# Performance work log

Measured on AMD Instinct MI355X. Metric: run time of the kernel, lower is better.

## Reference

```python
import jax, jax.numpy as jnp
import numpy as np

# atom_dict indices
N_IDX, CA_IDX, C_IDX = 0, 1, 2
O4P_IDX, C2P_IDX, C1P_IDX = 11, 14, 15
NA_REF_IDX = 15  # C1'
TOP_K = 30
NUM_RBF = 16
MAX_REL = 32
NUM_POLY = 3
B, L, A = 1, 512, 24


def setup_inputs() -> dict:
    key = jax.random.key(0)
    ks = jax.random.split(key, 8)
    X = 5.0 * jax.random.normal(ks[0], (B, L, A, 3), dtype=jnp.float32)
    mask = jnp.ones((B, L), dtype=jnp.float32)
    R_idx = jnp.broadcast_to(jnp.arange(L, dtype=jnp.int32), (B, L))
    chain_labels = jnp.broadcast_to((jnp.arange(L) // (L // 2)).astype(jnp.int32), (B, L))
    X_m = jnp.ones((B, L, A), dtype=jnp.float32)
    R_polymer_type = jax.random.randint(ks[1], (B, L), 0, NUM_POLY)
    protein_mask = (R_polymer_type == 0).astype(jnp.float32)
    dna_mask = (R_polymer_type == 1).astype(jnp.float32)
    rna_mask = (R_polymer_type == 2).astype(jnp.float32)
    TOTAL_ATOMS = A + 2
    edge_in = 2 * MAX_REL + 2  # placeholder; real edge_in below
    edge_in = NUM_RBF * TOTAL_ATOMS * TOTAL_ATOMS + 16  # 10832
    W_pos = 0.1 * jax.random.normal(ks[2], (16, 2 * MAX_REL + 2), dtype=jnp.float32)
    b_pos = 0.01 * jax.random.normal(ks[3], (16,), dtype=jnp.float32)
    W_edge = 0.02 * jax.random.normal(ks[4], (128, edge_in), dtype=jnp.float32)
    W_node = 0.1 * jax.random.normal(ks[5], (128, NUM_POLY), dtype=jnp.float32)
    gamma_e = jnp.ones((128,), jnp.float32); beta_e = jnp.zeros((128,), jnp.float32)
    gamma_n = jnp.ones((128,), jnp.float32); beta_n = jnp.zeros((128,), jnp.float32)
    return dict(X=X, mask=mask, R_idx=R_idx, chain_labels=chain_labels, X_m=X_m,
                protein_mask=protein_mask, dna_mask=dna_mask, rna_mask=rna_mask,
                R_polymer_type=R_polymer_type, W_pos=W_pos, b_pos=b_pos,
                W_edge=W_edge, W_node=W_node, gamma_e=gamma_e, beta_e=beta_e,
                gamma_n=gamma_n, beta_n=beta_n)


def _get_cb(n, ca, c, wa, wb, wc):
    b = ca - n
    cc = c - ca
    a = jnp.cross(b, cc)
    return wa * a + wb * b + wc * cc + ca


def _layernorm(x, g, b, eps=1e-5):
    m = x.mean(-1, keepdims=True)
    v = ((x - m) ** 2).mean(-1, keepdims=True)
    return (x - m) / jnp.sqrt(v + eps) * g + b


def _dist_topk(Xc, mask):
    # Xc: [B,L,3]
    mask2d = mask[:, None, :] * mask[:, :, None]  # [B,L,L]
    dX = Xc[:, None, :, :] - Xc[:, :, None, :]
    D = mask2d * jnp.sqrt((dX ** 2).sum(-1) + 1e-6)
    D_max = D.max(-1, keepdims=True)
    D_adjust = D + (1.0 - mask2d) * D_max
    negD, E_idx = jax.lax.top_k(-D_adjust, TOP_K)  # smallest distances
    return -negD, E_idx


def reference(X, mask, R_idx, chain_labels, X_m, protein_mask, dna_mask, rna_mask,
              R_polymer_type, W_pos, b_pos, W_edge, W_node, gamma_e, beta_e,
              gamma_n, beta_n):
    Bb, Ll = X.shape[0], X.shape[1]
    Ca = X[:, :, CA_IDX]
    Nb = X[:, :, N_IDX]
    Cc = X[:, :, C_IDX]
    Cb = _get_cb(Nb, Ca, Cc, -0.58273431, 0.56802827, -0.54067466)
    na_ref = X[:, :, NA_REF_IDX]
    N_na = _get_cb(X[:, :, O4P_IDX], X[:, :, C1P_IDX], X[:, :, C2P_IDX],
                   -0.56967352, 0.51055973, -0.53122153)
    aug_X = jnp.concatenate([X, Cb[:, :, None, :], N_na[:, :, None, :]], axis=2)  # [B,L,26,3]
    aug_Xm = jnp.concatenate([X_m, protein_mask[:, :, None],
                              (rna_mask + dna_mask)[:, :, None]], axis=-1)  # [B,L,26]

    _, E_idx = _dist_topk(Ca + na_ref, mask)  # [B,L,K]

    # gather neighbor atoms / masks: [B,L,K,26,3], [B,L,K,26]
    bidx = jnp.arange(Bb)[:, None, None]
    X_g = aug_X[bidx, E_idx]
    Xm_g = aug_Xm[bidx, E_idx]

    # all-atom pairwise distances [B,L,K,26,26]
    Dall = jnp.sqrt(((aug_X[:, :, None, :, None, :] - X_g[:, :, :, None, :, :]) ** 2).sum(-1) + 1e-6)
    D_mu = jnp.linspace(2.0, 22.0, NUM_RBF)
    D_sigma = (22.0 - 2.0) / NUM_RBF
    RBF = jnp.exp(-((Dall[..., None] - D_mu) / D_sigma) ** 2)  # [B,L,K,26,26,16]
    RBF = RBF * aug_Xm[:, :, None, :, None, None] * Xm_g[:, :, :, None, :, None]
    RBF_all = RBF.reshape(Bb, Ll, TOP_K, -1)  # [B,L,K,26*26*16]

    offset = R_idx[:, :, None] - R_idx[:, None, :]  # [B,L,L]
    offset = jnp.take_along_axis(offset, E_idx, axis=2)  # [B,L,K]
    d_chains = (chain_labels[:, :, None] == chain_labels[:, None, :]).astype(jnp.int32)
    E_chains = jnp.take_along_axis(d_chains, E_idx, axis=2)

    d = jnp.clip(offset + MAX_REL, 0, 2 * MAX_REL) * E_chains + (1 - E_chains) * (2 * MAX_REL + 1)
    d_onehot = jax.nn.one_hot(d, 2 * MAX_REL + 2, dtype=jnp.float32)
    E_positional = d_onehot @ W_pos.T + b_pos  # [B,L,K,16]

    E = jnp.concatenate([E_positional, RBF_all], axis=-1)
    E = E @ W_edge.T  # [B,L,K,128]
    E = _layernorm(E, gamma_e, beta_e)

    V = jax.nn.one_hot(R_polymer_type, NUM_POLY, dtype=jnp.float32) @ W_node.T
    V = _layernorm(V, gamma_n, beta_n)
    return V, E, E_idx
```

## Files before the change

kernel.cpp:

```cpp
#include <hip/hip_runtime.h>
#include <stdint.h>


#define NRES   512
#define TOPK   30
#define NATOM  26
#define KTOT   10832
#define NBLK128 85
#define MTOT   (NRES*TOPK)
#define NOUT   128
#define KSPLIT 4
#define TBINS  1024
#define TRANGE 25.6f

#define OFF_AUGX4  0u
#define OFF_EIDX   212992u
#define OFF_WSWZ   274432u
#define OFF_EPART  1667072u
#define OFF_TAB    25260032u

#define OUT_V     0
#define OUT_E     (NRES*NOUT)
#define OUT_EIDX  (OUT_E + MTOT*NOUT)

typedef __attribute__((ext_vector_type(4))) float f32x4;
typedef __attribute__((ext_vector_type(8))) int   i32x8;

#define SA_C    0.96089792702915984f
#define MU0_C   1.9217958540583197f
#define MUS_C   1.2811972360388798f
#define MUS2_C  (MUS_C*MUS_C)
#define SCL1    0x7f7f7f7f
#define TSCL    (SA_C * (float)TBINS / TRANGE)

__device__ __forceinline__ unsigned short f2bf(float f) {
    unsigned u = __builtin_bit_cast(unsigned, f);
    return (unsigned short)((u + 0x7fffu + ((u >> 16) & 1u)) >> 16);
}
__device__ __forceinline__ float bf2f(unsigned short u) {
    return __builtin_bit_cast(float, (unsigned)u << 16);
}
__device__ __forceinline__ float bflo(unsigned u) {
    return __builtin_bit_cast(float, u << 16);
}
__device__ __forceinline__ float bfhi(unsigned u) {
    return __builtin_bit_cast(float, u & 0xffff0000u);
}
__device__ __forceinline__ unsigned long long shfl_xor_u64(unsigned long long v, int m) {
    unsigned lo = (unsigned)v, hi = (unsigned)(v >> 32);
    lo = (unsigned)__shfl_xor((int)lo, m, 64);
    hi = (unsigned)__shfl_xor((int)hi, m, 64);
    return ((unsigned long long)hi << 32) | lo;
}
__device__ __forceinline__ float fexp2(float x) { return __builtin_amdgcn_exp2f(x); }
__device__ __forceinline__ float fsqrtf(float x) { return __builtin_amdgcn_sqrtf(x); }

__device__ __forceinline__ uint4 lut16(const uint4* __restrict__ tabS,
                                       float4 xi, float jx, float jy, float jz) {
    float dx = xi.x - jx, dy = xi.y - jy, dz = xi.z - jz;
    float d2 = __builtin_fmaf(dx, dx, __builtin_fmaf(dy, dy,
               __builtin_fmaf(dz, dz, 1e-6f)));
    float fi = fsqrtf(d2) * TSCL;
    fi = fminf(fi, (float)(TBINS - 1));
    return tabS[(int)fi];
}

__global__ __launch_bounds__(256) void kPrep(
    const float* __restrict__ X, const float* __restrict__ Xm,
    const float* __restrict__ prot, const float* __restrict__ dna,
    const float* __restrict__ rna, const int* __restrict__ ptype,
    const float* __restrict__ Wn, const float* __restrict__ gn,
    const float* __restrict__ bn, const float* __restrict__ We,
    char* __restrict__ ws, float* __restrict__ out)
{
    if (blockIdx.x >= NRES + 384) {
        int bb = (blockIdx.x - (NRES + 384)) * 256 + threadIdx.x;
        if (bb >= TBINS) return;
        float Ds = ((float)bb + 0.5f) * (TRANGE / (float)TBINS);
        unsigned r[4];
        #pragma unroll
        for (int g = 0; g < 4; g++) {
            float u0 = Ds - (MU0_C + (float)(4*g + 0) * MUS_C);
            float u1 = Ds - (MU0_C + (float)(4*g + 1) * MUS_C);
            float u2 = Ds - (MU0_C + (float)(4*g + 2) * MUS_C);
            float u3 = Ds - (MU0_C + (float)(4*g + 3) * MUS_C);
            float e0 = fexp2(-(u0 * u0));
            float e1 = fexp2(-(u1 * u1));
            float e2 = fexp2(-(u2 * u2));
            float e3 = fexp2(-(u3 * u3));
            int p = __builtin_amdgcn_cvt_pk_fp8_f32(e0, e1, 0, false);
            p     = __builtin_amdgcn_cvt_pk_fp8_f32(e2, e3, p, true);
            r[g] = (unsigned)p;
        }
        *(uint4*)(ws + OFF_TAB + (size_t)bb * 16) =
            make_uint4(r[0], r[1], r[2], r[3]);
        return;
    }
    if (blockIdx.x >= NRES) {
        int idx = blockIdx.x - NRES;
        int n = idx / 3;
        int s = (idx - n*3)*256 + threadIdx.x;
        if (s >= 677) return;
        const float* src = We + (size_t)n*KTOT + ((s < 676) ? (16 + s*16) : 0);
        float4 v0 = ((const float4*)src)[0];
        float4 v1 = ((const float4*)src)[1];
        float4 v2 = ((const float4*)src)[2];
        float4 v3 = ((const float4*)src)[3];
        int d = s >> 3, sl = s & 7, qd2 = sl >> 1, cc = sl & 1;
        size_t base = OFF_WSWZ
                    + (((size_t)(d*8 + (n >> 4))*64) + (size_t)(qd2*16 + (n & 15)))*32
                    + (size_t)cc*16;
        int r0 = __builtin_amdgcn_cvt_pk_fp8_f32(v0.x, v0.y, 0, false);
        r0     = __builtin_amdgcn_cvt_pk_fp8_f32(v0.z, v0.w, r0, true);
        int r1 = __builtin_amdgcn_cvt_pk_fp8_f32(v1.x, v1.y, 0, false);
        r1     = __builtin_amdgcn_cvt_pk_fp8_f32(v1.z, v1.w, r1, true);
        int r2 = __builtin_amdgcn_cvt_pk_fp8_f32(v2.x, v2.y, 0, false);
        r2     = __builtin_amdgcn_cvt_pk_fp8_f32(v2.z, v2.w, r2, true);
        int r3 = __builtin_amdgcn_cvt_pk_fp8_f32(v3.x, v3.y, 0, false);
        r3     = __builtin_amdgcn_cvt_pk_fp8_f32(v3.z, v3.w, r3, true);
        *(uint4*)(ws + base) = make_uint4((unsigned)r0, (unsigned)r1,
                                          (unsigned)r2, (unsigned)r3);
        return;
    }

    const int i = blockIdx.x, t = threadIdx.x;
    if (t >= 128) return;
    float4* augX4 = (float4*)(ws + OFF_AUGX4);
    int*    Eidx  = (int*)(ws + OFF_EIDX);
    const float* Xi = X + i * 72;

    if (t < 26) {
        float x, y, z, mk;
        if (t < 24) {
            x = Xi[t*3]; y = Xi[t*3+1]; z = Xi[t*3+2];
            mk = Xm[i*24 + t];
        } else if (t == 24) {
            float b0 = Xi[3]-Xi[0], b1 = Xi[4]-Xi[1], b2 = Xi[5]-Xi[2];
            float c0 = Xi[6]-Xi[3], c1 = Xi[7]-Xi[4], c2 = Xi[8]-Xi[5];
            float a0 = b1*c2-b2*c1, a1 = b2*c0-b0*c2, a2 = b0*c1-b1*c0;
            x = -0.58273431f*a0 + 0.56802827f*b0 - 0.54067466f*c0 + Xi[3];
            y = -0.58273431f*a1 + 0.56802827f*b1 - 0.54067466f*c1 + Xi[4];
            z = -0.58273431f*a2 + 0.56802827f*b2 - 0.54067466f*c2 + Xi[5];
            mk = prot[i];
        } else {
            const float* O4 = Xi + 33; const float* C1 = Xi + 45; const float* C2 = Xi + 42;
            float b0 = C1[0]-O4[0], b1 = C1[1]-O4[1], b2 = C1[2]-O4[2];
            float c0 = C2[0]-C1[0], c1 = C2[1]-C1[1], c2 = C2[2]-C1[2];
            float a0 = b1*c2-b2*c1, a1 = b2*c0-b0*c2, a2 = b0*c1-b1*c0;
            x = -0.56967352f*a0 + 0.51055973f*b0 - 0.53122153f*c0 + C1[0];
            y = -0.56967352f*a1 + 0.51055973f*b1 - 0.53122153f*c1 + C1[1];
            z = -0.56967352f*a2 + 0.51055973f*b2 - 0.53122153f*c2 + C1[2];
            mk = dna[i] + rna[i];
        }
        augX4[i*26 + t] = make_float4(x, y, z, mk);
    }

    __shared__ float red[4];
    int ty = ptype[i];
    float v = Wn[t*3 + ty];
    float s = v;
    #pragma unroll
    for (int off = 32; off; off >>= 1) s += __shfl_xor(s, off, 64);
    if ((t & 63) == 0) red[t>>6] = s;
    __syncthreads();
    float mean = (red[0] + red[1]) * (1.0f/128.0f);
    float d = v - mean;
    float s2 = d*d;
    #pragma unroll
    for (int off = 32; off; off >>= 1) s2 += __shfl_xor(s2, off, 64);
    if ((t & 63) == 0) red[2 + (t>>6)] = s2;
    __syncthreads();
    float var = (red[2] + red[3]) * (1.0f/128.0f);
    out[OUT_V + i*NOUT + t] = d * rsqrtf(var + 1e-5f) * gn[t] + bn[t];

    if (t >= 64) return;
    const int l = t;
    float xi0 = Xi[3] + Xi[45], xi1 = Xi[4] + Xi[46], xi2 = Xi[5] + Xi[47];
    unsigned long long cand[8];
    #pragma unroll
    for (int sg = 0; sg < 8; sg++) {
        int j = sg*64 + l;
        const float* Xj = X + j*72;
        float c0 = Xj[3] + Xj[45], c1 = Xj[4] + Xj[46], c2 = Xj[5] + Xj[47];
        float dx = xi0 - c0, dy = xi1 - c1, dz = xi2 - c2;
        float dd = __fadd_rn(__fadd_rn(__fadd_rn(__fmul_rn(dx,dx), __fmul_rn(dy,dy)),
                                       __fmul_rn(dz,dz)), 1e-6f);
        float D = sqrtf(dd);
        cand[sg] = ((unsigned long long)__builtin_bit_cast(unsigned, D) << 32) | (unsigned)j;
    }
    for (int m = 0; m < TOPK; m++) {
        unsigned long long k = cand[0];
        #pragma unroll
        for (int sg = 1; sg < 8; sg++) if (cand[sg] < k) k = cand[sg];
        #pragma unroll
        for (int off = 32; off; off >>= 1) {
            unsigned long long o = shfl_xor_u64(k, off);
            if (o < k) k = o;
        }
        if (l == 0) {
            int j = (int)(k & 0xffffffffu);
            Eidx[i*TOPK + m] = j;
            out[OUT_EIDX + i*TOPK + m] = (float)j;
        }
        #pragma unroll
        for (int sg = 0; sg < 8; sg++) if (cand[sg] == k) cand[sg] = ~0ull;
    }
}

__global__ __launch_bounds__(256, 4) void kC(const int* __restrict__ Ridx,
                                             const int* __restrict__ chain,
                                             const float* __restrict__ Wp,
                                             const float* __restrict__ bp,
                                             char* __restrict__ ws)
{
    const int bx = blockIdx.x, q = blockIdx.y;
    const int t = threadIdx.x, lane = t & 63, w = t >> 6;
    const int mlane = lane & 15, qd = lane >> 4;
    const int rtb = (w & 1) * 2;
    const int fg  = w >> 1;

    const float4* augX4 = (const float4*)(ws + OFF_AUGX4);
    const int*    Eidx  = (const int*)(ws + OFF_EIDX);
    unsigned short* Ep  = (unsigned short*)(ws + OFF_EPART)
                        + (size_t)q * MTOT * NOUT;

    __shared__ uint2  jT[NATOM * 65];
    __shared__ float4 iT[5 * 26];
    __shared__ int    JrowS[64];
    __shared__ uint4  tabS[TBINS];

    if (t < 64) JrowS[t] = Eidx[bx*64 + t];
    __syncthreads();
    const int i_base = (bx*64) / TOPK;
    if (t < 5*26) {
        int il_ = t / 26, aa = t - il_*26;
        int gi = i_base + il_; gi = gi > 511 ? 511 : gi;
        float4 v = augX4[(size_t)gi*26 + aa];
        if (v.w == 0.0f) { v.x = 30000.0f; v.y = 30000.0f; v.z = 30000.0f; }
        iT[t] = v;
    }
    {
        const uint4* tabG = (const uint4*)(ws + OFF_TAB);
        #pragma unroll
        for (int k = 0; k < 4; k++) tabS[t + k*256] = tabG[t + k*256];
    }
    for (int wk = t; wk < NATOM*64; wk += 256) {
        int aa = wk >> 6, rl_ = wk & 63;
        float4 p = augX4[(size_t)JrowS[rl_]*26 + aa];
        float x = p.x, y = p.y, z = p.z;
        if (p.w == 0.0f) { x = -30000.0f; y = -30000.0f; z = -30000.0f; }
        uint2 pk;
        pk.x = (unsigned)f2bf(x) | ((unsigned)f2bf(y) << 16);
        pk.y = (unsigned)f2bf(z);
        jT[aa*65 + rl_] = pk;
    }
    __syncthreads();

    int rl[2], il[2];
    #pragma unroll
    for (int rt = 0; rt < 2; rt++) {
        rl[rt] = (rtb + rt)*16 + mlane;
        il[rt] = ((bx*64 + rl[rt]) / TOPK - i_base) * 26;
    }

    f32x4 acc[2][4];
    #pragma unroll
    for (int rt = 0; rt < 2; rt++)
        #pragma unroll
        for (int nt = 0; nt < 4; nt++)
            acc[rt][nt] = (f32x4){0.f,0.f,0.f,0.f};

    const int d0 = (q == 0) ? 0 : (22 + (q-1)*21);
    const int nmain = (q == 0) ? 22 : ((q == 3) ? 20 : 21);

    int s0i = d0*8 + 2*qd;
    int a = s0i / 26, rem = s0i - a*26;

    const char* Wb = (const char*)(ws + OFF_WSWZ) + (size_t)d0*16384
                   + (size_t)(fg*4)*2048 + (size_t)lane*32;

    i32x8 b0 = *(const i32x8*)(Wb);
    i32x8 b1 = *(const i32x8*)(Wb + 2048);
    i32x8 b2 = *(const i32x8*)(Wb + 4096);
    i32x8 b3 = *(const i32x8*)(Wb + 6144);

    for (int dd = 0; dd < nmain; dd++) {
        i32x8 n0 = *(const i32x8*)(Wb + 16384);
        i32x8 n1 = *(const i32x8*)(Wb + 16384 + 2048);
        i32x8 n2 = *(const i32x8*)(Wb + 16384 + 4096);
        i32x8 n3 = *(const i32x8*)(Wb + 16384 + 6144);

        int rem1 = rem + 1, a1 = a;
        if (rem1 == 26) { rem1 = 0; a1 = a + 1; }

        #pragma unroll
        for (int rt = 0; rt < 2; rt++) {
            uint2 ja = jT[rem*65  + rl[rt]];
            uint2 jb = jT[rem1*65 + rl[rt]];
            float4 xa = iT[il[rt] + a];
            float4 xb = iT[il[rt] + a1];
            uint4 pa = lut16(tabS, xa, bflo(ja.x), bfhi(ja.x), bflo(ja.y));
            uint4 pb = lut16(tabS, xb, bflo(jb.x), bfhi(jb.x), bflo(jb.y));
            i32x8 A;
            A[0]=pa.x; A[1]=pa.y; A[2]=pa.z; A[3]=pa.w;
            A[4]=pb.x; A[5]=pb.y; A[6]=pb.z; A[7]=pb.w;
            __builtin_amdgcn_s_setprio(1);
            acc[rt][0] = __builtin_amdgcn_mfma_scale_f32_16x16x128_f8f6f4(A, b0, acc[rt][0], 0, 0, 0, SCL1, 0, SCL1);
            acc[rt][1] = __builtin_amdgcn_mfma_scale_f32_16x16x128_f8f6f4(A, b1, acc[rt][1], 0, 0, 0, SCL1, 0, SCL1);
            acc[rt][2] = __builtin_amdgcn_mfma_scale_f32_16x16x128_f8f6f4(A, b2, acc[rt][2], 0, 0, 0, SCL1, 0, SCL1);
            acc[rt][3] = __builtin_amdgcn_mfma_scale_f32_16x16x128_f8f6f4(A, b3, acc[rt][3], 0, 0, 0, SCL1, 0, SCL1);
            __builtin_amdgcn_s_setprio(0);
        }

        b0 = n0; b1 = n1; b2 = n2; b3 = n3;
        Wb += 16384;
        rem += 8;
        if (rem >= 26) { rem -= 26; a += 1; }
    }

    if (q == 3) {
        int rem1 = rem + 1, a1 = a;
        if (rem1 == 26) { rem1 = 0; a1 = a + 1; }
        int ac  = a  > 25 ? 25 : a;
        int a1c = a1 > 25 ? 25 : a1;

        int dcv[2];
        if (qd == 2) {
            #pragma unroll
            for (int rt = 0; rt < 2; rt++) {
                int j  = JrowS[rl[rt]];
                int i_ = (bx*64 + rl[rt]) / TOPK;
                int off  = Ridx[i_] - Ridx[j];
                int same = (chain[i_] == chain[j]);
                int dc = off + 32; dc = dc < 0 ? 0 : (dc > 64 ? 64 : dc);
                dcv[rt] = same ? dc : 65;
            }
        }

        #pragma unroll
        for (int rt = 0; rt < 2; rt++) {
            uint2 ja = jT[rem*65  + rl[rt]];
            uint2 jb = jT[rem1*65 + rl[rt]];
            float4 xa = iT[il[rt] + ac];
            float4 xb = iT[il[rt] + a1c];
            uint4 pa = lut16(tabS, xa, bflo(ja.x), bfhi(ja.x), bflo(ja.y));
            uint4 pb = lut16(tabS, xb, bflo(jb.x), bfhi(jb.x), bflo(jb.y));

            if (qd == 2) {
                float e[16];
                #pragma unroll
                for (int f = 0; f < 16; f++)
                    e[f] = Wp[f*66 + dcv[rt]] + bp[f];
                int u0 = __builtin_amdgcn_cvt_pk_fp8_f32(e[0], e[1], 0, false);
                u0     = __builtin_amdgcn_cvt_pk_fp8_f32(e[2], e[3], u0, true);
                int u1 = __builtin_amdgcn_cvt_pk_fp8_f32(e[4], e[5], 0, false);
                u1     = __builtin_amdgcn_cvt_pk_fp8_f32(e[6], e[7], u1, true);
                int u2 = __builtin_amdgcn_cvt_pk_fp8_f32(e[8], e[9], 0, false);
                u2     = __builtin_amdgcn_cvt_pk_fp8_f32(e[10], e[11], u2, true);
                int u3 = __builtin_amdgcn_cvt_pk_fp8_f32(e[12], e[13], 0, false);
                u3     = __builtin_amdgcn_cvt_pk_fp8_f32(e[14], e[15], u3, true);
                pa = make_uint4((unsigned)u0,(unsigned)u1,(unsigned)u2,(unsigned)u3);
                pb = make_uint4(0,0,0,0);
            }
            if (qd == 3) {
                pa = make_uint4(0,0,0,0);
                pb = make_uint4(0,0,0,0);
            }

            i32x8 A;
            A[0]=pa.x; A[1]=pa.y; A[2]=pa.z; A[3]=pa.w;
            A[4]=pb.x; A[5]=pb.y; A[6]=pb.z; A[7]=pb.w;
            __builtin_amdgcn_s_setprio(1);
            acc[rt][0] = __builtin_amdgcn_mfma_scale_f32_16x16x128_f8f6f4(A, b0, acc[rt][0], 0, 0, 0, SCL1, 0, SCL1);
            acc[rt][1] = __builtin_amdgcn_mfma_scale_f32_16x16x128_f8f6f4(A, b1, acc[rt][1], 0, 0, 0, SCL1, 0, SCL1);
            acc[rt][2] = __builtin_amdgcn_mfma_scale_f32_16x16x128_f8f6f4(A, b2, acc[rt][2], 0, 0, 0, SCL1, 0, SCL1);
            acc[rt][3] = __builtin_amdgcn_mfma_scale_f32_16x16x128_f8f6f4(A, b3, acc[rt][3], 0, 0, 0, SCL1, 0, SCL1);
            __builtin_amdgcn_s_setprio(0);
        }
    }

    #pragma unroll
    for (int rt = 0; rt < 2; rt++) {
        #pragma unroll
        for (int nt = 0; nt < 4; nt++) {
            int col = (fg*4 + nt)*16 + mlane;
            #pragma unroll
            for (int rr = 0; rr < 4; rr++) {
                int g0 = bx*64 + (rtb + rt)*16 + qd*4 + rr;
                Ep[(size_t)g0*NOUT + col] = f2bf(acc[rt][nt][rr]);
            }
        }
    }
}

__global__ __launch_bounds__(256) void kD(const float* __restrict__ ge,
                                          const float* __restrict__ be,
                                          char* __restrict__ ws,
                                          float* __restrict__ out)
{
    const uint2* Ep2 = (const uint2*)(ws + OFF_EPART);
    const int t = threadIdx.x, wv = t >> 6, lane = t & 63;
    const int half = lane >> 5, hl = lane & 31;
    const int row = blockIdx.x*8 + wv*2 + half;
    const size_t qs2 = (size_t)MTOT * 32;
    size_t b = (size_t)row*32 + hl;

    float v0 = 0.f, v1 = 0.f, v2 = 0.f, v3 = 0.f;
    #pragma unroll
    for (int qq = 0; qq < KSPLIT; qq++) {
        uint2 u = Ep2[b + (size_t)qq*qs2];
        v0 += bf2f((unsigned short)(u.x & 0xffffu));
        v1 += bf2f((unsigned short)(u.x >> 16));
        v2 += bf2f((unsigned short)(u.y & 0xffffu));
        v3 += bf2f((unsigned short)(u.y >> 16));
    }

    float S = v0 + v1 + v2 + v3;
    float Q = v0*v0 + v1*v1 + v2*v2 + v3*v3;
    #pragma unroll
    for (int off = 16; off; off >>= 1) {
        S += __shfl_xor(S, off, 64);
        Q += __shfl_xor(Q, off, 64);
    }
    float mean = S * (1.0f/128.0f);
    float var  = Q * (1.0f/128.0f) - mean*mean;
    float rstd = rsqrtf(var + 1e-5f);
    int c0 = hl*4;
    float4 o;
    o.x = (v0 - mean) * rstd * ge[c0]   + be[c0];
    o.y = (v1 - mean) * rstd * ge[c0+1] + be[c0+1];
    o.z = (v2 - mean) * rstd * ge[c0+2] + be[c0+2];
    o.w = (v3 - mean) * rstd * ge[c0+3] + be[c0+3];
    ((float4*)(out + OUT_E))[(size_t)row*32 + hl] = o;
}

extern "C" void kernel_launch(void* const* d_in, const int* in_sizes, int n_in,
                              void* d_out, int out_size, void* d_ws, size_t ws_size,
                              hipStream_t stream)
{
    const float* X     = (const float*)d_in[0];
    const int*   Ridx  = (const int*)d_in[2];
    const int*   chain = (const int*)d_in[3];
    const float* Xm    = (const float*)d_in[4];
    const float* prot  = (const float*)d_in[5];
    const float* dna   = (const float*)d_in[6];
    const float* rna   = (const float*)d_in[7];
    const int*   ptype = (const int*)d_in[8];
    const float* Wp    = (const float*)d_in[9];
    const float* bp    = (const float*)d_in[10];
    const float* We    = (const float*)d_in[11];
    const float* Wn    = (const float*)d_in[12];
    const float* ge    = (const float*)d_in[13];
    const float* be    = (const float*)d_in[14];
    const float* gn    = (const float*)d_in[15];
    const float* bn    = (const float*)d_in[16];
    char* ws = (char*)d_ws;
    float* out = (float*)d_out;

    kPrep<<<dim3(NRES + 384 + TBINS/256), dim3(256), 0, stream>>>(X, Xm, prot,
            dna, rna, ptype, Wn, gn, bn, We, ws, out);
    kC<<<dim3(240, KSPLIT), dim3(256), 0, stream>>>(Ridx, chain, Wp, bp, ws);
    kD<<<dim3(MTOT/8), dim3(256), 0, stream>>>(ge, be, ws, out);
}
```

Baseline: 150.6 us.

## Fuse split-K reduction and layernorm into GEMM kernel via last-block counter

Removes the separate reduce+layernorm kernel by having the last of the four split-K blocks for each row tile, found through an atomic counter, sum the bf16 partials and apply layernorm. The counters are zeroed by an extra block in the prep kernel. This drops one kernel launch and lets the reduction of early tiles overlap with GEMM work still running elsewhere, at the cost of fences, an atomic per block and a serialized tail in the last block. It also removes the s_setprio around the MFMA groups.

```diff
diff --git a/kernel.cpp b/kernel.cpp
--- a/kernel.cpp
+++ b/kernel.cpp
@@ -18,6 +18,7 @@
 #define OFF_WSWZ   274432u
 #define OFF_EPART  1667072u
 #define OFF_TAB    25260032u
+#define OFF_CNT    25276416u
 
 #define OUT_V     0
 #define OUT_E     (NRES*NOUT)
@@ -73,6 +74,10 @@
     const float* __restrict__ bn, const float* __restrict__ We,
     char* __restrict__ ws, float* __restrict__ out)
 {
+    if (blockIdx.x >= NRES + 384 + TBINS/256) {
+        if (threadIdx.x < 240) ((int*)(ws + OFF_CNT))[threadIdx.x] = 0;
+        return;
+    }
     if (blockIdx.x >= NRES + 384) {
         int bb = (blockIdx.x - (NRES + 384)) * 256 + threadIdx.x;
         if (bb >= TBINS) return;
@@ -211,7 +216,10 @@
                                              const int* __restrict__ chain,
                                              const float* __restrict__ Wp,
                                              const float* __restrict__ bp,
-                                             char* __restrict__ ws)
+                                             const float* __restrict__ ge,
+                                             const float* __restrict__ be,
+                                             char* __restrict__ ws,
+                                             float* __restrict__ out)
 {
     const int bx = blockIdx.x, q = blockIdx.y;
     const int t = threadIdx.x, lane = t & 63, w = t >> 6;
@@ -228,6 +236,7 @@
     __shared__ float4 iT[5 * 26];
     __shared__ int    JrowS[64];
     __shared__ uint4  tabS[TBINS];
+    __shared__ int    lastFlag;
 
     if (t < 64) JrowS[t] = Eidx[bx*64 + t];
     __syncthreads();
@@ -304,12 +313,10 @@
             i32x8 A;
             A[0]=pa.x; A[1]=pa.y; A[2]=pa.z; A[3]=pa.w;
             A[4]=pb.x; A[5]=pb.y; A[6]=pb.z; A[7]=pb.w;
-            __builtin_amdgcn_s_setprio(1);
             acc[rt][0] = __builtin_amdgcn_mfma_scale_f32_16x16x128_f8f6f4(A, b0, acc[rt][0], 0, 0, 0, SCL1, 0, SCL1);
             acc[rt][1] = __builtin_amdgcn_mfma_scale_f32_16x16x128_f8f6f4(A, b1, acc[rt][1], 0, 0, 0, SCL1, 0, SCL1);
             acc[rt][2] = __builtin_amdgcn_mfma_scale_f32_16x16x128_f8f6f4(A, b2, acc[rt][2], 0, 0, 0, SCL1, 0, SCL1);
             acc[rt][3] = __builtin_amdgcn_mfma_scale_f32_16x16x128_f8f6f4(A, b3, acc[rt][3], 0, 0, 0, SCL1, 0, SCL1);
-            __builtin_amdgcn_s_setprio(0);
         }
 
         b0 = n0; b1 = n1; b2 = n2; b3 = n3;
@@ -370,12 +377,10 @@
             i32x8 A;
             A[0]=pa.x; A[1]=pa.y; A[2]=pa.z; A[3]=pa.w;
             A[4]=pb.x; A[5]=pb.y; A[6]=pb.z; A[7]=pb.w;
-            __builtin_amdgcn_s_setprio(1);
             acc[rt][0] = __builtin_amdgcn_mfma_scale_f32_16x16x128_f8f6f4(A, b0, acc[rt][0], 0, 0, 0, SCL1, 0, SCL1);
             acc[rt][1] = __builtin_amdgcn_mfma_scale_f32_16x16x128_f8f6f4(A, b1, acc[rt][1], 0, 0, 0, SCL1, 0, SCL1);
             acc[rt][2] = __builtin_amdgcn_mfma_scale_f32_16x16x128_f8f6f4(A, b2, acc[rt][2], 0, 0, 0, SCL1, 0, SCL1);
             acc[rt][3] = __builtin_amdgcn_mfma_scale_f32_16x16x128_f8f6f4(A, b3, acc[rt][3], 0, 0, 0, SCL1, 0, SCL1);
-            __builtin_amdgcn_s_setprio(0);
         }
     }
 
@@ -391,47 +396,51 @@
             }
         }
     }
-}
-
-__global__ __launch_bounds__(256) void kD(const float* __restrict__ ge,
-                                          const float* __restrict__ be,
-                                          char* __restrict__ ws,
-                                          float* __restrict__ out)
-{
+
+    __threadfence();
+    __syncthreads();
+    if (t == 0) {
+        int old = atomicAdd((int*)(ws + OFF_CNT) + bx, 1);
+        lastFlag = (old == KSPLIT - 1);
+    }
+    __syncthreads();
+    if (!lastFlag) return;
+    __threadfence();
+
     const uint2* Ep2 = (const uint2*)(ws + OFF_EPART);
-    const int t = threadIdx.x, wv = t >> 6, lane = t & 63;
     const int half = lane >> 5, hl = lane & 31;
-    const int row = blockIdx.x*8 + wv*2 + half;
     const size_t qs2 = (size_t)MTOT * 32;
-    size_t b = (size_t)row*32 + hl;
-
-    float v0 = 0.f, v1 = 0.f, v2 = 0.f, v3 = 0.f;
-    #pragma unroll
-    for (int qq = 0; qq < KSPLIT; qq++) {
-        uint2 u = Ep2[b + (size_t)qq*qs2];
-        v0 += bf2f((unsigned short)(u.x & 0xffffu));
-        v1 += bf2f((unsigned short)(u.x >> 16));
-        v2 += bf2f((unsigned short)(u.y & 0xffffu));
-        v3 += bf2f((unsigned short)(u.y >> 16));
-    }
-
-    float S = v0 + v1 + v2 + v3;
-    float Q = v0*v0 + v1*v1 + v2*v2 + v3*v3;
-    #pragma unroll
-    for (int off = 16; off; off >>= 1) {
-        S += __shfl_xor(S, off, 64);
-        Q += __shfl_xor(Q, off, 64);
-    }
-    float mean = S * (1.0f/128.0f);
-    float var  = Q * (1.0f/128.0f) - mean*mean;
-    float rstd = rsqrtf(var + 1e-5f);
-    int c0 = hl*4;
-    float4 o;
-    o.x = (v0 - mean) * rstd * ge[c0]   + be[c0];
-    o.y = (v1 - mean) * rstd * ge[c0+1] + be[c0+1];
-    o.z = (v2 - mean) * rstd * ge[c0+2] + be[c0+2];
-    o.w = (v3 - mean) * rstd * ge[c0+3] + be[c0+3];
-    ((float4*)(out + OUT_E))[(size_t)row*32 + hl] = o;
+    #pragma unroll
+    for (int pass = 0; pass < 8; pass++) {
+        int row = bx*64 + pass*8 + w*2 + half;
+        size_t b = (size_t)row*32 + hl;
+        float v0 = 0.f, v1 = 0.f, v2 = 0.f, v3 = 0.f;
+        #pragma unroll
+        for (int qq = 0; qq < KSPLIT; qq++) {
+            uint2 u = Ep2[b + (size_t)qq*qs2];
+            v0 += bf2f((unsigned short)(u.x & 0xffffu));
+            v1 += bf2f((unsigned short)(u.x >> 16));
+            v2 += bf2f((unsigned short)(u.y & 0xffffu));
+            v3 += bf2f((unsigned short)(u.y >> 16));
+        }
+        float S = v0 + v1 + v2 + v3;
+        float Q = v0*v0 + v1*v1 + v2*v2 + v3*v3;
+        #pragma unroll
+        for (int off = 16; off; off >>= 1) {
+            S += __shfl_xor(S, off, 64);
+            Q += __shfl_xor(Q, off, 64);
+        }
+        float mean = S * (1.0f/128.0f);
+        float var  = Q * (1.0f/128.0f) - mean*mean;
+        float rstd = rsqrtf(var + 1e-5f);
+        int c0 = hl*4;
+        float4 o;
+        o.x = (v0 - mean) * rstd * ge[c0]   + be[c0];
+        o.y = (v1 - mean) * rstd * ge[c0+1] + be[c0+1];
+        o.z = (v2 - mean) * rstd * ge[c0+2] + be[c0+2];
+        o.w = (v3 - mean) * rstd * ge[c0+3] + be[c0+3];
+        ((float4*)(out + OUT_E))[(size_t)row*32 + hl] = o;
+    }
 }
 
 extern "C" void kernel_launch(void* const* d_in, const int* in_sizes, int n_in,
@@ -457,8 +466,8 @@
     char* ws = (char*)d_ws;
     float* out = (float*)d_out;
 
-    kPrep<<<dim3(NRES + 384 + TBINS/256), dim3(256), 0, stream>>>(X, Xm, prot,
-            dna, rna, ptype, Wn, gn, bn, We, ws, out);
-    kC<<<dim3(240, KSPLIT), dim3(256), 0, stream>>>(Ridx, chain, Wp, bp, ws);
-    kD<<<dim3(MTOT/8), dim3(256), 0, stream>>>(ge, be, ws, out);
-}
+    kPrep<<<dim3(NRES + 384 + TBINS/256 + 1), dim3(256), 0, stream>>>(X, Xm,
+            prot, dna, rna, ptype, Wn, gn, bn, We, ws, out);
+    kC<<<dim3(240, KSPLIT), dim3(256), 0, stream>>>(Ridx, chain, Wp, bp,
+            ge, be, ws, out);
+}
```

Result: slower. 309.1 us (+105.3%).
